# Optimization experiments

Hardware: AMD Instinct MI355X
Metric: run time of the kernel (lower is better)

The kernel has to match this reference:

```python
import jax, jax.numpy as jnp
import numpy as np

BS, T, D_IN, D_H, D_OUT = 8, 4096, 1024, 1024, 1024


def setup_inputs() -> dict:
    key = jax.random.key(0)
    kx, ka, kb, kc = jax.random.split(key, 4)
    x = jax.random.normal(kx, (BS, T, D_IN), dtype=jnp.float32)
    # stable_init: uniform in [0.999, 1.001)
    a = jax.random.uniform(ka, (D_H,), minval=0.999, maxval=1.001, dtype=jnp.float32)
    # glorot_normal: std = sqrt(2 / (fan_in + fan_out))
    b = jax.random.normal(kb, (D_IN, D_H), dtype=jnp.float32) * np.sqrt(2.0 / (D_IN + D_H))
    c = jax.random.normal(kc, (D_H, D_OUT), dtype=jnp.float32) * np.sqrt(2.0 / (D_H + D_OUT))
    return {"x": x, "a": a, "b": b, "c": c}


def reference(x, a, b, c):
    # Precompute input projection as one big GEMM: u[b,t,h] = x @ b  (input-independent of recurrence)
    u = jnp.einsum('bti,ih->bth', x, b)
    u = jnp.swapaxes(u, 0, 1)  # [T, BS, H] for scan over time

    def step(h, u_t):
        h = h * a + u_t  # diagonal linear recurrence
        return h, h

    init = jnp.zeros((x.shape[0], a.shape[0]), dtype=x.dtype)
    _, hs = jax.lax.scan(step, init, u)  # hs: [T, BS, H]
    # Output projection as one batched GEMM, then back to [BS, T, D_OUT]
    y = jnp.einsum('tbh,ho->bto', hs, c)
    return y
```

## Files before the change

kernel.cpp:

```cpp
#include <hip/hip_runtime.h>
#include <hip/hip_bf16.h>
#include <stdint.h>

#define BS 8
#define TT 4096
#define DI 1024
#define DH 1024
#define DO 1024
#define M1 (BS*TT)
#define NC 64
#define CL (TT/NC)

typedef __attribute__((ext_vector_type(8))) __bf16 bf16x8;
typedef __attribute__((ext_vector_type(4))) __bf16 bf16x4;
typedef __attribute__((ext_vector_type(4))) float f32x4;

__global__ void conv_bf16_kernel(const float* __restrict__ in, __bf16* __restrict__ out, int n8) {
    int i = blockIdx.x * blockDim.x + threadIdx.x;
    int stride = gridDim.x * blockDim.x;
    for (; i < n8; i += stride) {
        f32x4 v0 = *(const f32x4*)&in[(size_t)i * 8];
        f32x4 v1 = *(const f32x4*)&in[(size_t)i * 8 + 4];
        bf16x8 o;
        o[0] = (__bf16)v0[0]; o[1] = (__bf16)v0[1]; o[2] = (__bf16)v0[2]; o[3] = (__bf16)v0[3];
        o[4] = (__bf16)v1[0]; o[5] = (__bf16)v1[1]; o[6] = (__bf16)v1[2]; o[7] = (__bf16)v1[3];
        *(bf16x8*)&out[(size_t)i * 8] = o;
    }
}

__global__ void transp_conv_kernel(const float* __restrict__ src, __bf16* __restrict__ dst,
                                   int K, int N) {
    __shared__ float tile[32][33];
    const int tx = threadIdx.x & 31;
    const int ty = threadIdx.x >> 5;
    const int k0 = blockIdx.x * 32;
    const int n0 = blockIdx.y * 32;
    #pragma unroll
    for (int i = 0; i < 32; i += 8)
        tile[ty + i][tx] = src[(size_t)(k0 + ty + i) * N + n0 + tx];
    __syncthreads();
    #pragma unroll
    for (int i = 0; i < 32; i += 8)
        dst[(size_t)(n0 + ty + i) * K + k0 + tx] = (__bf16)tile[tx][ty + i];
}

template<int OUTF32>
__global__ __launch_bounds__(512, 2) void gemm256_kernel(
    const __bf16* __restrict__ A, const __bf16* __restrict__ Bt,
    __bf16* __restrict__ Obf, float* __restrict__ Of,
    int M, int N, int K)
{
    __shared__ __bf16 lds[65536];
    const int tid = threadIdx.x;
    const int wv = tid >> 6;
    const int l  = tid & 63;
    const int sr = wv >> 2;
    const int sc = wv & 3;
    const int lr = l & 15;
    const int lk = (l >> 4) * 8;
    const int xsw = (lr & 7) * 8;
    const int ak0 = lk ^ xsw, ak1 = (32 + lk) ^ xsw;
    const int rowBase = blockIdx.x * 256;
    const int colBase = blockIdx.y * 256;
    const int aOff = (sr * 64 + lr) * 64;
    const int bOff = (sc * 32 + lr) * 64;
    const int csw = ((l & 7) ^ (l >> 3)) * 8;
    const __bf16* aSrc0 = A  + (size_t)(rowBase + wv * 16 + (l >> 3)) * K + csw;
    const __bf16* bSrc0 = Bt + (size_t)(colBase + wv * 16 + (l >> 3)) * K + csw;

    f32x4 acc[2][2][4][2];
    #pragma unroll
    for (int a0 = 0; a0 < 2; a0++)
        #pragma unroll
        for (int b0 = 0; b0 < 2; b0++)
            #pragma unroll
            for (int m = 0; m < 4; m++)
                #pragma unroll
                for (int n = 0; n < 2; n++)
                    acc[a0][b0][m][n] = (f32x4){0.f, 0.f, 0.f, 0.f};

    bf16x8 aF0[4][2], aF1[4][2], bF[2][2];

#define GLD(s, d) __builtin_amdgcn_global_load_lds( \
        (const __attribute__((address_space(1))) void*)(s), \
        (__attribute__((address_space(3))) void*)(d), 16, 0, 0)
#define STAGE_A(buf, half, ktE) do { \
        const __bf16* s_ = aSrc0 + (size_t)(half) * 128 * K + (ktE); \
        __bf16* d_ = &lds[((buf) * 2 + (half)) * 8192 + wv * 1024]; \
        GLD(s_, d_); GLD(s_ + (size_t)8 * K, d_ + 512); } while (0)
#define STAGE_B(buf, half, ktE) do { \
        const __bf16* s_ = bSrc0 + (size_t)(half) * 128 * K + (ktE); \
        __bf16* d_ = &lds[32768 + ((buf) * 2 + (half)) * 8192 + wv * 1024]; \
        GLD(s_, d_); GLD(s_ + (size_t)8 * K, d_ + 512); } while (0)
#define LOADA(buf, qr, AF) do { \
        const __bf16* Ab_ = &lds[((buf) * 2 + (qr)) * 8192 + aOff]; \
        _Pragma("unroll") \
        for (int m = 0; m < 4; m++) { \
            AF[m][0] = *(const bf16x8*)&Ab_[m * 1024 + ak0]; \
            AF[m][1] = *(const bf16x8*)&Ab_[m * 1024 + ak1]; } } while (0)
#define LOADB(buf, qc) do { \
        const __bf16* Bb_ = &lds[32768 + ((buf) * 2 + (qc)) * 8192 + bOff]; \
        _Pragma("unroll") \
        for (int n = 0; n < 2; n++) { \
            bF[n][0] = *(const bf16x8*)&Bb_[n * 1024 + ak0]; \
            bF[n][1] = *(const bf16x8*)&Bb_[n * 1024 + ak1]; } } while (0)
#define MMQ(qr, qc, AF) do { \
        __builtin_amdgcn_s_setprio(1); \
        _Pragma("unroll") \
        for (int m = 0; m < 4; m++) \
            _Pragma("unroll") \
            for (int n = 0; n < 2; n++) { \
                acc[qr][qc][m][n] = __builtin_amdgcn_mfma_f32_16x16x32_bf16(AF[m][0], bF[n][0], acc[qr][qc][m][n], 0, 0, 0); \
                acc[qr][qc][m][n] = __builtin_amdgcn_mfma_f32_16x16x32_bf16(AF[m][1], bF[n][1], acc[qr][qc][m][n], 0, 0, 0); } \
        __builtin_amdgcn_s_setprio(0); } while (0)
#define PH_BAR() do { __builtin_amdgcn_sched_barrier(0); __builtin_amdgcn_s_barrier(); \
        asm volatile("s_waitcnt lgkmcnt(0)" ::: "memory"); \
        __builtin_amdgcn_sched_barrier(0); } while (0)
#define PHEND() do { __builtin_amdgcn_sched_barrier(0); __builtin_amdgcn_s_barrier(); } while (0)
#define PHEND_W(cond) do { __builtin_amdgcn_sched_barrier(0); \
        if (cond) { asm volatile("s_waitcnt vmcnt(0)" ::: "memory"); } \
        else      { asm volatile("s_waitcnt vmcnt(4)" ::: "memory"); } \
        __builtin_amdgcn_s_barrier(); } while (0)

    const int NIT = K >> 7;

    STAGE_A(0, 0, 0); STAGE_A(0, 1, 0); STAGE_B(0, 0, 0); STAGE_B(0, 1, 0);
    STAGE_A(1, 0, 64); STAGE_A(1, 1, 64); STAGE_B(1, 0, 64); STAGE_B(1, 1, 64);
    asm volatile("s_waitcnt vmcnt(8)" ::: "memory");
    __builtin_amdgcn_s_barrier();

    for (int it = 0; it < NIT; ++it) {
        const int ktOdd  = (2 * it + 1) * 64;
        const int ktEv2  = (2 * it + 2) * 64;
        const int ktOdd2 = (2 * it + 3) * 64;
        const bool last = (it == NIT - 1);
        LOADA(0, 0, aF0); LOADB(0, 0);
        if (it > 0) STAGE_A(1, 1, ktOdd);
        PH_BAR(); MMQ(0, 0, aF0); PHEND();
        LOADA(0, 1, aF1);
        if (it > 0) STAGE_B(1, 1, ktOdd);
        PH_BAR(); MMQ(1, 0, aF1); PHEND();
        LOADB(0, 1);
        if (!last) STAGE_B(0, 0, ktEv2);
        PH_BAR(); MMQ(1, 1, aF1); PHEND();
        if (!last) STAGE_A(0, 0, ktEv2);
        PH_BAR(); MMQ(0, 1, aF0); PHEND_W(last);
        LOADA(1, 0, aF0); LOADB(1, 0);
        if (!last) STAGE_A(0, 1, ktEv2);
        PH_BAR(); MMQ(0, 0, aF0); PHEND();
        LOADA(1, 1, aF1);
        if (!last) STAGE_B(0, 1, ktEv2);
        PH_BAR(); MMQ(1, 0, aF1); PHEND();
        LOADB(1, 1);
        if (!last) STAGE_B(1, 0, ktOdd2);
        PH_BAR(); MMQ(1, 1, aF1); PHEND();
        if (!last) STAGE_A(1, 0, ktOdd2);
        PH_BAR(); MMQ(0, 1, aF0); PHEND_W(last);
    }

    #pragma unroll
    for (int qr = 0; qr < 2; qr++)
        #pragma unroll
        for (int qc = 0; qc < 2; qc++)
            #pragma unroll
            for (int m = 0; m < 4; m++)
                #pragma unroll
                for (int n = 0; n < 2; n++)
                    #pragma unroll
                    for (int j = 0; j < 4; j++) {
                        int row = rowBase + qr * 128 + sr * 64 + m * 16 + (l >> 4) * 4 + j;
                        int col = colBase + qc * 128 + sc * 32 + n * 16 + lr;
                        size_t idx = (size_t)row * N + col;
                        if constexpr (OUTF32) Of[idx] = acc[qr][qc][m][n][j];
                        else                  Obf[idx] = (__bf16)acc[qr][qc][m][n][j];
                    }
#undef GLD
#undef STAGE_A
#undef STAGE_B
#undef LOADA
#undef LOADB
#undef MMQ
#undef PH_BAR
#undef PHEND
#undef PHEND_W
}

__global__ void scan1_kernel(const __bf16* __restrict__ u, const float* __restrict__ a,
                             float* __restrict__ E) {
    int g = blockIdx.x * blockDim.x + threadIdx.x;
    int c4 = g & 255;
    int rest = g >> 8;
    int k = rest & (NC - 1);
    int b = rest >> 6;
    int ch = c4 * 4;
    f32x4 av = { a[ch], a[ch + 1], a[ch + 2], a[ch + 3] };
    size_t base = ((size_t)(b * TT + k * CL)) * DH + ch;
    f32x4 h = {0.f, 0.f, 0.f, 0.f};
    for (int t = 0; t < CL; t++) {
        bf16x4 v = *(const bf16x4*)&u[base + (size_t)t * DH];
        h[0] = h[0] * av[0] + (float)v[0];
        h[1] = h[1] * av[1] + (float)v[1];
        h[2] = h[2] * av[2] + (float)v[2];
        h[3] = h[3] * av[3] + (float)v[3];
    }
    *(f32x4*)&E[((size_t)(b * NC + k)) * DH + ch] = h;
}

__global__ void scan2_kernel(const float* __restrict__ E, const float* __restrict__ a,
                             float* __restrict__ Cc) {
    int g = blockIdx.x * blockDim.x + threadIdx.x;
    int ch = g & (DH - 1);
    int b = g >> 10;
    float av = a[ch];
    float aL = av;
    #pragma unroll
    for (int i = 0; i < 6; i++) aL *= aL;
    float carry = 0.f;
    for (int k = 0; k < NC; k++) {
        size_t idx = ((size_t)(b * NC + k)) * DH + ch;
        Cc[idx] = carry;
        carry = aL * carry + E[idx];
    }
}

__global__ void scan3_kernel(__bf16* __restrict__ u, const float* __restrict__ a,
                             const float* __restrict__ Cc) {
    int g = blockIdx.x * blockDim.x + threadIdx.x;
    int c4 = g & 255;
    int rest = g >> 8;
    int k = rest & (NC - 1);
    int b = rest >> 6;
    int ch = c4 * 4;
    f32x4 av = { a[ch], a[ch + 1], a[ch + 2], a[ch + 3] };
    f32x4 p = *(const f32x4*)&Cc[((size_t)(b * NC + k)) * DH + ch];
    f32x4 h = {0.f, 0.f, 0.f, 0.f};
    size_t base = ((size_t)(b * TT + k * CL)) * DH + ch;
    for (int t = 0; t < CL; t++) {
        size_t idx = base + (size_t)t * DH;
        bf16x4 v = *(bf16x4*)&u[idx];
        h[0] = h[0] * av[0] + (float)v[0];
        h[1] = h[1] * av[1] + (float)v[1];
        h[2] = h[2] * av[2] + (float)v[2];
        h[3] = h[3] * av[3] + (float)v[3];
        p[0] *= av[0]; p[1] *= av[1]; p[2] *= av[2]; p[3] *= av[3];
        bf16x4 o;
        o[0] = (__bf16)(h[0] + p[0]);
        o[1] = (__bf16)(h[1] + p[1]);
        o[2] = (__bf16)(h[2] + p[2]);
        o[3] = (__bf16)(h[3] + p[3]);
        *(bf16x4*)&u[idx] = o;
    }
}

extern "C" void kernel_launch(void* const* d_in, const int* in_sizes, int n_in,
                              void* d_out, int out_size, void* d_ws, size_t ws_size,
                              hipStream_t stream) {
    const float* x = (const float*)d_in[0];
    const float* a = (const float*)d_in[1];
    const float* b = (const float*)d_in[2];
    const float* c = (const float*)d_in[3];
    float* y = (float*)d_out;

    char* ws = (char*)d_ws;
    size_t off = 0;
    __bf16* u  = (__bf16*)(ws + off); off += (size_t)M1 * DH * 2;
    __bf16* bT = (__bf16*)(ws + off); off += (size_t)DI * DH * 2;
    __bf16* cT = (__bf16*)(ws + off); off += (size_t)DH * DO * 2;
    if (ws_size < off) return;

    __bf16* xbf = (__bf16*)d_out;
    float*  E   = (float*)((char*)d_out + (size_t)M1 * DI * 2);
    float*  Cc  = E + (size_t)BS * NC * DH;

    conv_bf16_kernel<<<2048, 256, 0, stream>>>(x, xbf, (M1 * DI) / 8);
    transp_conv_kernel<<<dim3(DI / 32, DH / 32), 256, 0, stream>>>(b, bT, DI, DH);
    transp_conv_kernel<<<dim3(DH / 32, DO / 32), 256, 0, stream>>>(c, cT, DH, DO);
    gemm256_kernel<0><<<dim3(M1 / 256, DH / 256), 512, 0, stream>>>(xbf, bT, u, nullptr, M1, DH, DI);
    scan1_kernel<<<(BS * NC * (DH / 4)) / 256, 256, 0, stream>>>(u, a, E);
    scan2_kernel<<<(BS * DH) / 256, 256, 0, stream>>>(E, a, Cc);
    scan3_kernel<<<(BS * NC * (DH / 4)) / 256, 256, 0, stream>>>(u, a, Cc);
    gemm256_kernel<1><<<dim3(M1 / 256, DO / 256), 512, 0, stream>>>(u, cT, nullptr, y, M1, DO, DH);
}
```

Measured before the change: 225.1 us.

## Restructure GEMM main loop to overlap LDS fragment reads with MFMA

Rewrites the GEMM k-loop into a GROUP macro that issues LDS fragment loads for the next quadrant (and the next buffer's A/B fragments) before the current MFMA block. It uses partial lgkmcnt waits instead of draining LDS before every MFMA phase, and double-buffers the B0 fragment registers. The loop is also hardcoded for K=1024 with a reordered quadrant traversal. This aims to hide LDS latency behind matrix-core work. In exchange it raises register pressure and relies on exact waitcnt counts, which makes it fragile.

```diff
diff --git a/kernel.cpp b/kernel.cpp
--- a/kernel.cpp
+++ b/kernel.cpp
@@ -79,7 +79,7 @@
                 for (int n = 0; n < 2; n++)
                     acc[a0][b0][m][n] = (f32x4){0.f, 0.f, 0.f, 0.f};
 
-    bf16x8 aF0[4][2], aF1[4][2], bF[2][2];
+    bf16x8 a0f[4][2], a1f[4][2], b0a[2][2], b0b[2][2], b1f[2][2];
 
 #define GLD(s, d) __builtin_amdgcn_global_load_lds( \
         (const __attribute__((address_space(1))) void*)(s), \
@@ -98,65 +98,67 @@
         for (int m = 0; m < 4; m++) { \
             AF[m][0] = *(const bf16x8*)&Ab_[m * 1024 + ak0]; \
             AF[m][1] = *(const bf16x8*)&Ab_[m * 1024 + ak1]; } } while (0)
-#define LOADB(buf, qc) do { \
+#define LOADB(buf, qc, BF) do { \
         const __bf16* Bb_ = &lds[32768 + ((buf) * 2 + (qc)) * 8192 + bOff]; \
         _Pragma("unroll") \
         for (int n = 0; n < 2; n++) { \
-            bF[n][0] = *(const bf16x8*)&Bb_[n * 1024 + ak0]; \
-            bF[n][1] = *(const bf16x8*)&Bb_[n * 1024 + ak1]; } } while (0)
-#define MMQ(qr, qc, AF) do { \
+            BF[n][0] = *(const bf16x8*)&Bb_[n * 1024 + ak0]; \
+            BF[n][1] = *(const bf16x8*)&Bb_[n * 1024 + ak1]; } } while (0)
+#define MMQ(qr, qc, AF, BF) do { \
         __builtin_amdgcn_s_setprio(1); \
         _Pragma("unroll") \
         for (int m = 0; m < 4; m++) \
             _Pragma("unroll") \
             for (int n = 0; n < 2; n++) { \
-                acc[qr][qc][m][n] = __builtin_amdgcn_mfma_f32_16x16x32_bf16(AF[m][0], bF[n][0], acc[qr][qc][m][n], 0, 0, 0); \
-                acc[qr][qc][m][n] = __builtin_amdgcn_mfma_f32_16x16x32_bf16(AF[m][1], bF[n][1], acc[qr][qc][m][n], 0, 0, 0); } \
+                acc[qr][qc][m][n] = __builtin_amdgcn_mfma_f32_16x16x32_bf16(AF[m][0], BF[n][0], acc[qr][qc][m][n], 0, 0, 0); \
+                acc[qr][qc][m][n] = __builtin_amdgcn_mfma_f32_16x16x32_bf16(AF[m][1], BF[n][1], acc[qr][qc][m][n], 0, 0, 0); } \
         __builtin_amdgcn_s_setprio(0); } while (0)
-#define PH_BAR() do { __builtin_amdgcn_sched_barrier(0); __builtin_amdgcn_s_barrier(); \
-        asm volatile("s_waitcnt lgkmcnt(0)" ::: "memory"); \
-        __builtin_amdgcn_sched_barrier(0); } while (0)
-#define PHEND() do { __builtin_amdgcn_sched_barrier(0); __builtin_amdgcn_s_barrier(); } while (0)
-#define PHEND_W(cond) do { __builtin_amdgcn_sched_barrier(0); \
-        if (cond) { asm volatile("s_waitcnt vmcnt(0)" ::: "memory"); } \
-        else      { asm volatile("s_waitcnt vmcnt(4)" ::: "memory"); } \
-        __builtin_amdgcn_s_barrier(); } while (0)
-
-    const int NIT = K >> 7;
+#define SB __builtin_amdgcn_sched_barrier(0)
+#define BAR __builtin_amdgcn_s_barrier()
+#define LGKM(n) asm volatile("s_waitcnt lgkmcnt(" #n ")" ::: "memory")
+
+#define GROUP(buf, kt, B0CUR, B0NXT, STG, RDN) do { \
+     \
+    LOADB(buf, 1, b1f); \
+    if (STG) STAGE_A(buf, 0, (kt) + 128); \
+    SB; BAR; LGKM(4); SB; \
+    MMQ(0, 0, a0f, B0CUR); \
+    SB; BAR; \
+     \
+    LOADA(buf, 1, a1f); \
+    if (STG) STAGE_B(buf, 0, (kt) + 128); \
+    SB; BAR; LGKM(8); SB; \
+    MMQ(0, 1, a0f, b1f); \
+    SB; asm volatile("s_waitcnt vmcnt(4)" ::: "memory"); BAR; \
+     \
+    if (RDN) LOADA(1 - (buf), 0, a0f); \
+    if (STG) STAGE_B(buf, 1, (kt) + 128); \
+    SB; BAR; \
+    if (RDN) { LGKM(8); } else { LGKM(0); } \
+    SB; \
+    MMQ(1, 1, a1f, b1f); \
+    SB; BAR; \
+     \
+    if (RDN) LOADB(1 - (buf), 0, B0NXT); \
+    if (STG) STAGE_A(buf, 1, (kt) + 128); \
+    SB; BAR; SB; \
+    MMQ(1, 0, a1f, B0CUR); \
+    SB; LGKM(0); BAR; \
+} while (0)
 
     STAGE_A(0, 0, 0); STAGE_A(0, 1, 0); STAGE_B(0, 0, 0); STAGE_B(0, 1, 0);
     STAGE_A(1, 0, 64); STAGE_A(1, 1, 64); STAGE_B(1, 0, 64); STAGE_B(1, 1, 64);
     asm volatile("s_waitcnt vmcnt(8)" ::: "memory");
-    __builtin_amdgcn_s_barrier();
-
-    for (int it = 0; it < NIT; ++it) {
-        const int ktOdd  = (2 * it + 1) * 64;
-        const int ktEv2  = (2 * it + 2) * 64;
-        const int ktOdd2 = (2 * it + 3) * 64;
-        const bool last = (it == NIT - 1);
-        LOADA(0, 0, aF0); LOADB(0, 0);
-        if (it > 0) STAGE_A(1, 1, ktOdd);
-        PH_BAR(); MMQ(0, 0, aF0); PHEND();
-        LOADA(0, 1, aF1);
-        if (it > 0) STAGE_B(1, 1, ktOdd);
-        PH_BAR(); MMQ(1, 0, aF1); PHEND();
-        LOADB(0, 1);
-        if (!last) STAGE_B(0, 0, ktEv2);
-        PH_BAR(); MMQ(1, 1, aF1); PHEND();
-        if (!last) STAGE_A(0, 0, ktEv2);
-        PH_BAR(); MMQ(0, 1, aF0); PHEND_W(last);
-        LOADA(1, 0, aF0); LOADB(1, 0);
-        if (!last) STAGE_A(0, 1, ktEv2);
-        PH_BAR(); MMQ(0, 0, aF0); PHEND();
-        LOADA(1, 1, aF1);
-        if (!last) STAGE_B(0, 1, ktEv2);
-        PH_BAR(); MMQ(1, 0, aF1); PHEND();
-        LOADB(1, 1);
-        if (!last) STAGE_B(1, 0, ktOdd2);
-        PH_BAR(); MMQ(1, 1, aF1); PHEND();
-        if (!last) STAGE_A(1, 0, ktOdd2);
-        PH_BAR(); MMQ(0, 1, aF0); PHEND_W(last);
-    }
+    BAR;
+    LOADA(0, 0, a0f); LOADB(0, 0, b0a);
+    SB; LGKM(0); SB; BAR;
+
+    for (int it = 0; it < 7; ++it) {
+        GROUP(0, it * 128,      b0a, b0b, 1, 1);
+        GROUP(1, it * 128 + 64, b0b, b0a, 1, 1);
+    }
+    GROUP(0, 896, b0a, b0b, 0, 1);
+    GROUP(1, 960, b0b, b0a, 0, 0);
 
     #pragma unroll
     for (int qr = 0; qr < 2; qr++)
@@ -180,9 +182,10 @@
 #undef LOADA
 #undef LOADB
 #undef MMQ
-#undef PH_BAR
-#undef PHEND
-#undef PHEND_W
+#undef SB
+#undef BAR
+#undef LGKM
+#undef GROUP
 }
 
 __global__ void scan1_kernel(const __bf16* __restrict__ u, const float* __restrict__ a,
```

Result: slower. 322.8 us (+43.4%).

## Fuse chunk-local scan reduction into first GEMM epilogue

Applied to the files above, without the earlier changes.

Removes the separate scan1 pass by computing each 64-step chunk's end state, a weighted sum of a^(63-t)*u_t, directly from the GEMM accumulators in registers, using a wave shuffle reduction. This avoids re-reading the full bf16 u tensor from memory for the chunk sums. It adds epilogue ALU work and register pressure to the GEMM. It also sums fp32 accumulators rather than bf16-rounded u, which changes rounding slightly.

```diff
diff --git a/kernel.cpp b/kernel.cpp
--- a/kernel.cpp
+++ b/kernel.cpp
@@ -48,6 +48,7 @@
 __global__ __launch_bounds__(512, 2) void gemm256_kernel(
     const __bf16* __restrict__ A, const __bf16* __restrict__ Bt,
     __bf16* __restrict__ Obf, float* __restrict__ Of,
+    const float* __restrict__ Ea, float* __restrict__ Ep,
     int M, int N, int K)
 {
     __shared__ __bf16 lds[65536];
@@ -174,6 +175,43 @@
                         if constexpr (OUTF32) Of[idx] = acc[qr][qc][m][n][j];
                         else                  Obf[idx] = (__bf16)acc[qr][qc][m][n][j];
                     }
+
+    if constexpr (!OUTF32) {
+        const int hi = l >> 4;
+        const int bb = rowBase >> 12;
+        #pragma unroll
+        for (int qr = 0; qr < 2; qr++) {
+            const int r0 = rowBase + qr * 128 + sr * 64;
+            const int kch = (r0 & (TT - 1)) >> 6;
+            #pragma unroll
+            for (int qc = 0; qc < 2; qc++)
+                #pragma unroll
+                for (int n = 0; n < 2; n++) {
+                    const int ch = colBase + qc * 128 + sc * 32 + n * 16 + lr;
+                    const float av = Ea[ch];
+                    const float a2 = av * av, a4 = a2 * a2;
+                    const float a12 = a4 * a4 * a4;
+                    float w = 1.f;
+                    if (hi < 3) w *= a4;
+                    if (hi < 2) w *= a4;
+                    if (hi < 1) w *= a4;
+                    float e = 0.f;
+                    #pragma unroll
+                    for (int m = 3; m >= 0; --m) {
+                        #pragma unroll
+                        for (int j = 3; j >= 0; --j) {
+                            e += w * acc[qr][qc][m][n][j];
+                            w *= av;
+                        }
+                        w *= a12;
+                    }
+                    e += __shfl_xor(e, 16);
+                    e += __shfl_xor(e, 32);
+                    if (hi == 0)
+                        Ep[((size_t)(bb * NC + kch)) * DH + ch] = e;
+                }
+        }
+    }
 #undef GLD
 #undef STAGE_A
 #undef STAGE_B
@@ -183,27 +221,6 @@
 #undef PH_BAR
 #undef PHEND
 #undef PHEND_W
-}
-
-__global__ void scan1_kernel(const __bf16* __restrict__ u, const float* __restrict__ a,
-                             float* __restrict__ E) {
-    int g = blockIdx.x * blockDim.x + threadIdx.x;
-    int c4 = g & 255;
-    int rest = g >> 8;
-    int k = rest & (NC - 1);
-    int b = rest >> 6;
-    int ch = c4 * 4;
-    f32x4 av = { a[ch], a[ch + 1], a[ch + 2], a[ch + 3] };
-    size_t base = ((size_t)(b * TT + k * CL)) * DH + ch;
-    f32x4 h = {0.f, 0.f, 0.f, 0.f};
-    for (int t = 0; t < CL; t++) {
-        bf16x4 v = *(const bf16x4*)&u[base + (size_t)t * DH];
-        h[0] = h[0] * av[0] + (float)v[0];
-        h[1] = h[1] * av[1] + (float)v[1];
-        h[2] = h[2] * av[2] + (float)v[2];
-        h[3] = h[3] * av[3] + (float)v[3];
-    }
-    *(f32x4*)&E[((size_t)(b * NC + k)) * DH + ch] = h;
 }
 
 __global__ void scan2_kernel(const float* __restrict__ E, const float* __restrict__ a,
@@ -275,9 +292,8 @@
     conv_bf16_kernel<<<2048, 256, 0, stream>>>(x, xbf, (M1 * DI) / 8);
     transp_conv_kernel<<<dim3(DI / 32, DH / 32), 256, 0, stream>>>(b, bT, DI, DH);
     transp_conv_kernel<<<dim3(DH / 32, DO / 32), 256, 0, stream>>>(c, cT, DH, DO);
-    gemm256_kernel<0><<<dim3(M1 / 256, DH / 256), 512, 0, stream>>>(xbf, bT, u, nullptr, M1, DH, DI);
-    scan1_kernel<<<(BS * NC * (DH / 4)) / 256, 256, 0, stream>>>(u, a, E);
+    gemm256_kernel<0><<<dim3(M1 / 256, DH / 256), 512, 0, stream>>>(xbf, bT, u, nullptr, a, E, M1, DH, DI);
     scan2_kernel<<<(BS * DH) / 256, 256, 0, stream>>>(E, a, Cc);
     scan3_kernel<<<(BS * NC * (DH / 4)) / 256, 256, 0, stream>>>(u, a, Cc);
-    gemm256_kernel<1><<<dim3(M1 / 256, DO / 256), 512, 0, stream>>>(u, cT, nullptr, y, M1, DO, DH);
-}
+    gemm256_kernel<1><<<dim3(M1 / 256, DO / 256), 512, 0, stream>>>(u, cT, nullptr, y, nullptr, nullptr, M1, DO, DH);
+}
```

Measured after the change: 218.8 us, median of 2. 2.8% less time.
